# Performance work log

Hardware: AMD Instinct MI355X
Metric: run time of the kernel (lower is better)

The kernel has to match this reference:

```python
import jax, jax.numpy as jnp
import numpy as np

NUM_GRAPHS = 1024
BN_EPS = 1e-5
NEG_SLOPE = 0.01


def _xavier(key, fan_in, fan_out):
    lim = float(np.sqrt(6.0 / (fan_in + fan_out)))
    return jax.random.uniform(key, (fan_in, fan_out), jnp.float32, -lim, lim)


def setup_inputs() -> dict:
    key = jax.random.key(0)
    ks = jax.random.split(key, 10)
    N, F, H, C, E = 100000, 128, 128, 10, 1600000
    x = jax.random.normal(ks[0], (N, F), jnp.float32)
    edge_index = jax.random.randint(ks[1], (2, E), 0, N, jnp.int64)
    batch = jnp.sort(jax.random.randint(ks[2], (N,), 0, NUM_GRAPHS, jnp.int64))
    return {
        "x": x,
        "W1a": _xavier(ks[3], F, H), "b1a": jnp.zeros((H,), jnp.float32),
        "W1b": _xavier(ks[4], H, H), "b1b": jnp.zeros((H,), jnp.float32),
        "g1": jnp.ones((H,), jnp.float32), "be1": jnp.zeros((H,), jnp.float32),
        "W2a": _xavier(ks[5], H, H), "b2a": jnp.zeros((H,), jnp.float32),
        "W2b": _xavier(ks[6], H, H), "b2b": jnp.zeros((H,), jnp.float32),
        "g2": jnp.ones((H,), jnp.float32), "be2": jnp.zeros((H,), jnp.float32),
        "fcW1": _xavier(ks[7], H, H), "fcb1": jnp.zeros((H,), jnp.float32),
        "fcW2": _xavier(ks[8], H, C), "fcb2": jnp.zeros((C,), jnp.float32),
        "edge_index": edge_index,
        "batch": batch,
    }


def _leaky(x):
    return jax.nn.leaky_relu(x, NEG_SLOPE)


def _gin_conv(x, src, dst, Wa, ba, Wb, bb, num_nodes):
    # scatter-add neighbor aggregation: out[i] = (1+eps)*x[i] + sum_{j->i} x[j], eps=0
    agg = jax.ops.segment_sum(x[src], dst, num_segments=num_nodes)
    h = x + agg
    h = _leaky(h @ Wa + ba)
    return h @ Wb + bb


def _batch_norm(x, gamma, beta):
    # training-mode BN over node dim (biased variance, as torch BatchNorm1d)
    m = jnp.mean(x, axis=0)
    v = jnp.mean(jnp.square(x - m), axis=0)
    return gamma * (x - m) * jax.lax.rsqrt(v + BN_EPS) + beta


def reference(x, W1a, b1a, W1b, b1b, g1, be1, W2a, b2a, W2b, b2b, g2, be2,
              fcW1, fcb1, fcW2, fcb2, edge_index, batch):
    N = x.shape[0]
    src, dst = edge_index[0], edge_index[1]
    h = _leaky(_gin_conv(x, src, dst, W1a, b1a, W1b, b1b, N))
    h = _batch_norm(h, g1, be1)
    h = _leaky(_gin_conv(h, src, dst, W2a, b2a, W2b, b2b, N))
    h = _batch_norm(h, g2, be2)
    # global_add_pool: segment-sum nodes into graphs
    hg = jax.ops.segment_sum(h, batch, num_segments=NUM_GRAPHS)  # [G, H]
    hg = _leaky(hg @ fcW1 + fcb1)
    logits = hg @ fcW2 + fcb2
    return jax.nn.log_softmax(logits, axis=-1)
```

## Files before the change

kernel.cpp:

```cpp
#include <hip/hip_runtime.h>
#include <hip/hip_bf16.h>

#define NUM_GRAPHS 1024
#define NCLS 10
#define BN_EPS 1e-5f
#define SLOPE 0.01f
#define PB 256
#define WN 64
#define CAP 1280
#define NBMAX 1600

typedef __attribute__((ext_vector_type(8))) short          bfrag;
typedef __attribute__((ext_vector_type(4))) float          ffrag;
typedef __attribute__((ext_vector_type(8))) unsigned short ushort8;

__device__ __forceinline__ float leaky(float v) { return v > 0.f ? v : SLOPE * v; }

__device__ __forceinline__ unsigned short f2bf(float f) {
    unsigned int u = __float_as_uint(f);
    unsigned int r = (u + 0x7fffu + ((u >> 16) & 1u)) >> 16;
    return (unsigned short)r;
}
__device__ __forceinline__ float bf2f(unsigned short u) {
    return __uint_as_float(((unsigned int)u) << 16);
}

__device__ __forceinline__ void load_lds16(const void* g, void* l) {
    __builtin_amdgcn_global_load_lds((const __attribute__((address_space(1))) void*)g,
                                     (__attribute__((address_space(3))) void*)l, 16, 0, 0);
}

__global__ __launch_bounds__(256)
void scatter_cvt_kernel(const int* __restrict__ src, const int* __restrict__ dst,
                        int* __restrict__ cursor, int* __restrict__ packedE,
                        int E, int chunk, int NB,
                        const float* __restrict__ x, unsigned short* __restrict__ xb, int nX,
                        const float* __restrict__ W0, const float* __restrict__ W1,
                        const float* __restrict__ W2, const float* __restrict__ W3,
                        unsigned short* __restrict__ WT)
{
    int b = blockIdx.x;
    int t = threadIdx.x;
    if (b < PB) {
        __shared__ int h[NBMAX];
        __shared__ int base[NBMAX];
        for (int i = t; i < NB; i += 256) h[i] = 0;
        __syncthreads();
        int e0 = b * chunk;
        int e1 = min(E, e0 + chunk);
        for (int e = e0 + t; e < e1; e += 256)
            atomicAdd(&h[dst[e] >> 6], 1);
        __syncthreads();
        for (int i = t; i < NB; i += 256) {
            int c = h[i];
            base[i] = c ? atomicAdd(&cursor[i], c) : 0;
            h[i] = 0;
        }
        __syncthreads();
        for (int e = e0 + t; e < e1; e += 256) {
            int d = dst[e];
            int s = src[e];
            int bk = d >> 6;
            int off = atomicAdd(&h[bk], 1) + base[bk];
            if (off < CAP) packedE[bk * CAP + off] = (s << 6) | (d & 63);
        }
        return;
    }
    b -= PB;
    if (b < 4) {
        const float* W = (b == 0) ? W0 : (b == 1) ? W1 : (b == 2) ? W2 : W3;
        unsigned short* O = WT + (size_t)b * 16384;
#pragma unroll
        for (int p = 0; p < 64; ++p) {
            int idx = p * 256 + t;
            int n = idx >> 7, k = idx & 127;
            O[n * 128 + k] = f2bf(W[k * 128 + n]);
        }
        return;
    }
    b -= 4;
    int i = (b * 256 + t) * 4;
    if (i + 3 < nX) {
        float4 f = *(const float4*)&x[i];
        unsigned short o0 = f2bf(f.x), o1 = f2bf(f.y), o2 = f2bf(f.z), o3 = f2bf(f.w);
        unsigned long long packed = (unsigned long long)o0 | ((unsigned long long)o1 << 16)
                                  | ((unsigned long long)o2 << 32) | ((unsigned long long)o3 << 48);
        *(unsigned long long*)&xb[i] = packed;
    } else if (i < nX) {
        for (int j = i; j < nX; ++j) xb[j] = f2bf(x[j]);
    }
}

template<bool AFFINE>
__global__ __launch_bounds__(256)
void gather_win(const unsigned short* __restrict__ X, const int* __restrict__ cursor,
                const int* __restrict__ packedE,
                const float* __restrict__ bnsum, const float* __restrict__ bnsq,
                const float* __restrict__ g, const float* __restrict__ be,
                unsigned short* __restrict__ out, int N)
{
    __shared__ int   raw[CAP];
    __shared__ int   lst[CAP];
    __shared__ int   hist[WN];
    __shared__ int   offs[WN];
    __shared__ int   cur[WN];
    __shared__ float Af[128], Bf[128];

    const int k    = blockIdx.x >> 1;
    const int half = blockIdx.x & 1;
    const int t = threadIdx.x;

    if (t < WN) hist[t] = 0;
    if (AFFINE && t < 128) {
        float invN = 1.f / (float)N;
        float mean = bnsum[t] * invN;
        float var  = bnsq[t] * invN - mean * mean;
        float a = g[t] * rsqrtf(var + BN_EPS);
        Af[t] = a;
        Bf[t] = be[t] - a * mean;
    }
    __syncthreads();

    int cnt = cursor[k];
    if (cnt > CAP) cnt = CAP;
    const int* pe = packedE + (size_t)k * CAP;
    for (int i = t; i < cnt; i += 256) {
        int p = pe[i];
        raw[i] = p;
        atomicAdd(&hist[p & 63], 1);
    }
    __syncthreads();
    if (t < 64) {
        int v = hist[t];
        int x = v;
#pragma unroll
        for (int off = 1; off < 64; off <<= 1) {
            int y = __shfl_up(x, off, 64);
            if (t >= off) x += y;
        }
        offs[t] = x - v;
        cur[t]  = x - v;
    }
    __syncthreads();
    for (int i = t; i < cnt; i += 256) {
        int p = raw[i];
        int slot = atomicAdd(&cur[p & 63], 1);
        lst[slot] = p >> 6;
    }
    __syncthreads();

    const int grp = t >> 4;
    const int c8  = (t & 15) * 8;
#pragma unroll
    for (int pass = 0; pass < 2; ++pass) {
        int n = half * 32 + pass * 16 + grp;
        int node = k * WN + n;
        if (node >= N) continue;
        float acc[8];
        {
            ushort8 xv = *(const ushort8*)&X[(size_t)node * 128 + c8];
#pragma unroll
            for (int j = 0; j < 8; ++j) acc[j] = bf2f(xv[j]);
        }
        int s0 = offs[n];
        int dg = hist[n];
        int s1 = s0 + dg;
        int i = s0;
        for (; i + 1 < s1; i += 2) {
            int j0 = lst[i], j1 = lst[i + 1];
            ushort8 u0 = *(const ushort8*)&X[(size_t)j0 * 128 + c8];
            ushort8 u1 = *(const ushort8*)&X[(size_t)j1 * 128 + c8];
#pragma unroll
            for (int j = 0; j < 8; ++j) acc[j] += bf2f(u0[j]) + bf2f(u1[j]);
        }
        if (i < s1) {
            int j0 = lst[i];
            ushort8 u0 = *(const ushort8*)&X[(size_t)j0 * 128 + c8];
#pragma unroll
            for (int j = 0; j < 8; ++j) acc[j] += bf2f(u0[j]);
        }
        ushort8 o;
        if (AFFINE) {
            float cf = (float)(dg + 1);
#pragma unroll
            for (int j = 0; j < 8; ++j)
                o[j] = f2bf(fmaf(Af[c8 + j], acc[j], cf * Bf[c8 + j]));
        } else {
#pragma unroll
            for (int j = 0; j < 8; ++j) o[j] = f2bf(acc[j]);
        }
        *(ushort8*)&out[(size_t)node * 128 + c8] = o;
    }
}

template<bool STATS>
__global__ __launch_bounds__(256)
void gemm_mfma(const unsigned short* __restrict__ A, const unsigned short* __restrict__ WT,
               const float* __restrict__ bias, unsigned short* __restrict__ Out,
               float* __restrict__ stat_sum, float* __restrict__ stat_sq,
               const unsigned short* __restrict__ zeroPad, int N)
{
    __shared__ unsigned short As[128 * 128];
    __shared__ unsigned short Ws[128 * 128];
    __shared__ float sred[256];

    const int t = threadIdx.x;
    const int row0 = blockIdx.x * 128;

#pragma unroll
    for (int p = 0; p < 8; ++p) {
        int s  = p * 256 + t;
        int r  = s >> 4;
        int gp = s & 15;
        int g  = gp ^ (r & 7);
        int gr = row0 + r;
        const unsigned short* ga = (gr < N) ? &A[(size_t)gr * 128 + g * 8] : zeroPad;
        load_lds16(ga, &As[s * 8]);
        load_lds16(&WT[r * 128 + g * 8], &Ws[s * 8]);
    }
    __syncthreads();

    const int wave = t >> 6;
    const int lane = t & 63;
    const int m    = lane & 15;
    const int quad = lane >> 4;

    ffrag acc[2][8];
#pragma unroll
    for (int rt = 0; rt < 2; ++rt)
#pragma unroll
        for (int ct = 0; ct < 8; ++ct) {
            ffrag z = {0.f, 0.f, 0.f, 0.f};
            acc[rt][ct] = z;
        }

#pragma unroll
    for (int ks = 0; ks < 4; ++ks) {
        int kc = ks * 4 + quad;
        bfrag b[8];
#pragma unroll
        for (int ct = 0; ct < 8; ++ct) {
            int n = ct * 16 + m;
            b[ct] = *(const bfrag*)&Ws[(n * 16 + (kc ^ (n & 7))) * 8];
        }
        bfrag a0, a1;
        {
            int r = wave * 32 + m;
            a0 = *(const bfrag*)&As[(r * 16 + (kc ^ (r & 7))) * 8];
        }
        {
            int r = wave * 32 + 16 + m;
            a1 = *(const bfrag*)&As[(r * 16 + (kc ^ (r & 7))) * 8];
        }
#pragma unroll
        for (int ct = 0; ct < 8; ++ct) {
            acc[0][ct] = __builtin_amdgcn_mfma_f32_16x16x32_bf16(a0, b[ct], acc[0][ct], 0, 0, 0);
            acc[1][ct] = __builtin_amdgcn_mfma_f32_16x16x32_bf16(a1, b[ct], acc[1][ct], 0, 0, 0);
        }
    }

    float bv[8];
#pragma unroll
    for (int ct = 0; ct < 8; ++ct) bv[ct] = bias[ct * 16 + m];

    float colsum[8], colsq[8];
#pragma unroll
    for (int ct = 0; ct < 8; ++ct) { colsum[ct] = 0.f; colsq[ct] = 0.f; }

    __syncthreads();
    unsigned short* tw = &As[wave * 32 * 128];
#pragma unroll
    for (int rt = 0; rt < 2; ++rt) {
#pragma unroll
        for (int reg = 0; reg < 4; ++reg) {
            int rl = rt * 16 + quad * 4 + reg;
            bool valid = (row0 + wave * 32 + rl) < N;
#pragma unroll
            for (int ct = 0; ct < 8; ++ct) {
                float v = leaky(acc[rt][ct][reg] + bv[ct]);
                tw[rl * 128 + ct * 16 + m] = f2bf(v);
                if (STATS && valid) { colsum[ct] += v; colsq[ct] += v * v; }
            }
        }
    }
    __syncthreads();
#pragma unroll
    for (int p = 0; p < 8; ++p) {
        int li = p * 64 + lane;
        int rl = li >> 4;
        int cg = (li & 15) * 8;
        int r = row0 + wave * 32 + rl;
        if (r < N)
            *(ushort8*)&Out[(size_t)r * 128 + cg] = *(const ushort8*)&tw[rl * 128 + cg];
    }

    if (STATS) {
        __syncthreads();
        if (t < 128) { sred[t] = 0.f; sred[128 + t] = 0.f; }
        __syncthreads();
#pragma unroll
        for (int ct = 0; ct < 8; ++ct) {
            atomicAdd(&sred[ct * 16 + m], colsum[ct]);
            atomicAdd(&sred[128 + ct * 16 + m], colsq[ct]);
        }
        __syncthreads();
        if (t < 128) {
            atomicAdd(&stat_sum[t], sred[t]);
            atomicAdd(&stat_sq[t], sred[128 + t]);
        }
    }
}

__device__ __forceinline__ int lower_bound(const int* b, int n, int v)
{
    int lo = 0, hi = n;
    while (lo < hi) { int mid = (lo + hi) >> 1; if (b[mid] < v) lo = mid + 1; else hi = mid; }
    return lo;
}

__global__ __launch_bounds__(128)
void pool_head(const unsigned short* __restrict__ Hn, const int* __restrict__ batch,
               const float* __restrict__ bnsum, const float* __restrict__ bnsq,
               const float* __restrict__ g2, const float* __restrict__ be2,
               const float* __restrict__ fcW1, const float* __restrict__ fcb1,
               const float* __restrict__ fcW2, const float* __restrict__ fcb2,
               float* __restrict__ out, int N)
{
    int g = blockIdx.x;
    int t = threadIdx.x;
    __shared__ int bounds[2];
    __shared__ float row[128];
    __shared__ float z1[128];
    if (t < 2) bounds[t] = lower_bound(batch, N, g + t);
    float invN = 1.f / (float)N;
    float mean = bnsum[t] * invN;
    float var  = bnsq[t] * invN - mean * mean;
    float a2 = g2[t] * rsqrtf(var + BN_EPS);
    float b2 = be2[t] - a2 * mean;
    __syncthreads();
    int ss = bounds[0], se = bounds[1];
    float acc = 0.f;
    for (int i = ss; i < se; ++i) acc += bf2f(Hn[(size_t)i * 128 + t]);
    float cnt = (float)(se - ss);
    row[t] = fmaf(a2, acc, cnt * b2);
    __syncthreads();
    float a1 = fcb1[t];
#pragma unroll 8
    for (int k = 0; k < 128; ++k) a1 = fmaf(row[k], fcW1[(size_t)k * 128 + t], a1);
    z1[t] = leaky(a1);
    __syncthreads();
    if (t < 64) {
        float lg[NCLS];
#pragma unroll
        for (int c = 0; c < NCLS; ++c) {
            float p = z1[t] * fcW2[t * NCLS + c] + z1[t + 64] * fcW2[(t + 64) * NCLS + c];
#pragma unroll
            for (int off = 32; off > 0; off >>= 1) p += __shfl_down(p, off, 64);
            if (t == 0) lg[c] = p + fcb2[c];
        }
        if (t == 0) {
            float m = lg[0];
#pragma unroll
            for (int c = 1; c < NCLS; ++c) m = fmaxf(m, lg[c]);
            float s = 0.f;
#pragma unroll
            for (int c = 0; c < NCLS; ++c) s += expf(lg[c] - m);
            float lse = logf(s);
#pragma unroll
            for (int c = 0; c < NCLS; ++c) out[(size_t)g * NCLS + c] = lg[c] - m - lse;
        }
    }
}

extern "C" void kernel_launch(void* const* d_in, const int* in_sizes, int n_in,
                              void* d_out, int out_size, void* d_ws, size_t ws_size,
                              hipStream_t stream)
{
    const float* x    = (const float*)d_in[0];
    const float* W1a  = (const float*)d_in[1];
    const float* b1a  = (const float*)d_in[2];
    const float* W1b  = (const float*)d_in[3];
    const float* b1b  = (const float*)d_in[4];
    const float* g1   = (const float*)d_in[5];
    const float* be1  = (const float*)d_in[6];
    const float* W2a  = (const float*)d_in[7];
    const float* b2a  = (const float*)d_in[8];
    const float* W2b  = (const float*)d_in[9];
    const float* b2b  = (const float*)d_in[10];
    const float* g2   = (const float*)d_in[11];
    const float* be2  = (const float*)d_in[12];
    const float* fcW1 = (const float*)d_in[13];
    const float* fcb1 = (const float*)d_in[14];
    const float* fcW2 = (const float*)d_in[15];
    const float* fcb2 = (const float*)d_in[16];
    const int*   edge = (const int*)d_in[17];
    const int*   batch= (const int*)d_in[18];

    const int N = in_sizes[0] / 128;
    const int E = in_sizes[17] / 2;
    const int* src = edge;
    const int* dst = edge + E;
    const size_t NH = (size_t)N * 128;
    const int NB = (N + WN - 1) / WN;
    const int chunk = (E + PB - 1) / PB;

    int*   cursor = (int*)d_ws;
    float* stats  = (float*)(cursor + 2048);
    float* sum1   = stats;
    float* sq1    = stats + 128;
    float* sum2   = stats + 256;
    float* sq2    = stats + 384;
    unsigned short* zeroPad = (unsigned short*)(stats + 512);
    int*   packedE = (int*)(stats + 640);
    unsigned short* xb   = (unsigned short*)(packedE + ((size_t)NBMAX * CAP));
    unsigned short* bufA = xb + NH;
    unsigned short* bufB = bufA + NH;
    unsigned short* wt   = bufB + NH;
    unsigned short* wt1a = wt;
    unsigned short* wt1b = wt + 16384;
    unsigned short* wt2a = wt + 32768;
    unsigned short* wt2b = wt + 49152;

    const int cvtBlocks  = (int)((NH / 4 + 255) / 256);
    const int gemmBlocks = (N + 127) / 128;

    hipMemsetAsync(d_ws, 0, 2048 * sizeof(int) + 640 * sizeof(float), stream);

    scatter_cvt_kernel<<<PB + 4 + cvtBlocks, 256, 0, stream>>>(
        src, dst, cursor, packedE, E, chunk, NB,
        x, xb, (int)NH, W1a, W1b, W2a, W2b, wt);

    gather_win<false><<<NB * 2, 256, 0, stream>>>(xb, cursor, packedE,
                                                  nullptr, nullptr, nullptr, nullptr, bufA, N);
    gemm_mfma<false><<<gemmBlocks, 256, 0, stream>>>(bufA, wt1a, b1a, bufB,
                                                     nullptr, nullptr, zeroPad, N);
    gemm_mfma<true><<<gemmBlocks, 256, 0, stream>>>(bufB, wt1b, b1b, bufA,
                                                    sum1, sq1, zeroPad, N);

    gather_win<true><<<NB * 2, 256, 0, stream>>>(bufA, cursor, packedE,
                                                 sum1, sq1, g1, be1, bufB, N);
    gemm_mfma<false><<<gemmBlocks, 256, 0, stream>>>(bufB, wt2a, b2a, bufA,
                                                     nullptr, nullptr, zeroPad, N);
    gemm_mfma<true><<<gemmBlocks, 256, 0, stream>>>(bufA, wt2b, b2b, bufB,
                                                    sum2, sq2, zeroPad, N);

    pool_head<<<NUM_GRAPHS, 128, 0, stream>>>(bufB, batch, sum2, sq2, g2, be2,
                                              fcW1, fcb1, fcW2, fcb2, (float*)d_out, N);
}
```

Measured before the change: 434.1 us.

## Fuse both GIN MLP GEMMs into one kernel keeping the hidden tile in LDS

Each GIN conv's two 128x128 GEMMs now run in one kernel. The leaky-ReLU output of the first GEMM is written back, swizzled, into the A tile in shared memory and reused directly as the input of the second GEMM. This removes one global write and one global read of the N x 128 bf16 intermediate per conv, plus one kernel launch per conv. In exchange, LDS per block grows with a second weight tile, which lowers how many blocks fit per CU, and some barriers are dropped on the assumption that each wave only touches its own rows.

Measured after the change: 455.9 us. +5.0%, slower.

```diff
diff --git a/kernel.cpp b/kernel.cpp
--- a/kernel.cpp
+++ b/kernel.cpp
@@ -193,15 +193,17 @@
     }
 }
 
-template<bool STATS>
 __global__ __launch_bounds__(256)
-void gemm_mfma(const unsigned short* __restrict__ A, const unsigned short* __restrict__ WT,
-               const float* __restrict__ bias, unsigned short* __restrict__ Out,
-               float* __restrict__ stat_sum, float* __restrict__ stat_sq,
-               const unsigned short* __restrict__ zeroPad, int N)
+void conv_fused(const unsigned short* __restrict__ A,
+                const unsigned short* __restrict__ WT1, const float* __restrict__ b1,
+                const unsigned short* __restrict__ WT2, const float* __restrict__ b2,
+                unsigned short* __restrict__ Out,
+                float* __restrict__ stat_sum, float* __restrict__ stat_sq,
+                const unsigned short* __restrict__ zeroPad, int N)
 {
     __shared__ unsigned short As[128 * 128];
-    __shared__ unsigned short Ws[128 * 128];
+    __shared__ unsigned short W1s[128 * 128];
+    __shared__ unsigned short W2s[128 * 128];
     __shared__ float sred[256];
 
     const int t = threadIdx.x;
@@ -216,7 +218,8 @@
         int gr = row0 + r;
         const unsigned short* ga = (gr < N) ? &A[(size_t)gr * 128 + g * 8] : zeroPad;
         load_lds16(ga, &As[s * 8]);
-        load_lds16(&WT[r * 128 + g * 8], &Ws[s * 8]);
+        load_lds16(&WT1[r * 128 + g * 8], &W1s[s * 8]);
+        load_lds16(&WT2[r * 128 + g * 8], &W2s[s * 8]);
     }
     __syncthreads();
 
@@ -241,7 +244,7 @@
 #pragma unroll
         for (int ct = 0; ct < 8; ++ct) {
             int n = ct * 16 + m;
-            b[ct] = *(const bfrag*)&Ws[(n * 16 + (kc ^ (n & 7))) * 8];
+            b[ct] = *(const bfrag*)&W1s[(n * 16 + (kc ^ (n & 7))) * 8];
         }
         bfrag a0, a1;
         {
@@ -259,15 +262,65 @@
         }
     }
 
+    {
+        float bv[8];
+#pragma unroll
+        for (int ct = 0; ct < 8; ++ct) bv[ct] = b1[ct * 16 + m];
+#pragma unroll
+        for (int rt = 0; rt < 2; ++rt) {
+#pragma unroll
+            for (int reg = 0; reg < 4; ++reg) {
+                int rl = wave * 32 + rt * 16 + quad * 4 + reg;
+#pragma unroll
+                for (int ct = 0; ct < 8; ++ct) {
+                    int c = ct * 16 + m;
+                    float v = leaky(acc[rt][ct][reg] + bv[ct]);
+                    As[(rl * 16 + ((c >> 3) ^ (rl & 7))) * 8 + (c & 7)] = f2bf(v);
+                }
+            }
+        }
+    }
+
+#pragma unroll
+    for (int rt = 0; rt < 2; ++rt)
+#pragma unroll
+        for (int ct = 0; ct < 8; ++ct) {
+            ffrag z = {0.f, 0.f, 0.f, 0.f};
+            acc[rt][ct] = z;
+        }
+#pragma unroll
+    for (int ks = 0; ks < 4; ++ks) {
+        int kc = ks * 4 + quad;
+        bfrag b[8];
+#pragma unroll
+        for (int ct = 0; ct < 8; ++ct) {
+            int n = ct * 16 + m;
+            b[ct] = *(const bfrag*)&W2s[(n * 16 + (kc ^ (n & 7))) * 8];
+        }
+        bfrag a0, a1;
+        {
+            int r = wave * 32 + m;
+            a0 = *(const bfrag*)&As[(r * 16 + (kc ^ (r & 7))) * 8];
+        }
+        {
+            int r = wave * 32 + 16 + m;
+            a1 = *(const bfrag*)&As[(r * 16 + (kc ^ (r & 7))) * 8];
+        }
+#pragma unroll
+        for (int ct = 0; ct < 8; ++ct) {
+            acc[0][ct] = __builtin_amdgcn_mfma_f32_16x16x32_bf16(a0, b[ct], acc[0][ct], 0, 0, 0);
+            acc[1][ct] = __builtin_amdgcn_mfma_f32_16x16x32_bf16(a1, b[ct], acc[1][ct], 0, 0, 0);
+        }
+    }
+
     float bv[8];
 #pragma unroll
-    for (int ct = 0; ct < 8; ++ct) bv[ct] = bias[ct * 16 + m];
+    for (int ct = 0; ct < 8; ++ct) bv[ct] = b2[ct * 16 + m];
 
     float colsum[8], colsq[8];
 #pragma unroll
     for (int ct = 0; ct < 8; ++ct) { colsum[ct] = 0.f; colsq[ct] = 0.f; }
 
-    __syncthreads();
     unsigned short* tw = &As[wave * 32 * 128];
 #pragma unroll
     for (int rt = 0; rt < 2; ++rt) {
@@ -279,11 +332,10 @@
             for (int ct = 0; ct < 8; ++ct) {
                 float v = leaky(acc[rt][ct][reg] + bv[ct]);
                 tw[rl * 128 + ct * 16 + m] = f2bf(v);
-                if (STATS && valid) { colsum[ct] += v; colsq[ct] += v * v; }
+                if (valid) { colsum[ct] += v; colsq[ct] += v * v; }
             }
         }
     }
-    __syncthreads();
 #pragma unroll
     for (int p = 0; p < 8; ++p) {
         int li = p * 64 + lane;
@@ -294,20 +346,18 @@
             *(ushort8*)&Out[(size_t)r * 128 + cg] = *(const ushort8*)&tw[rl * 128 + cg];
     }
 
-    if (STATS) {
-        __syncthreads();
-        if (t < 128) { sred[t] = 0.f; sred[128 + t] = 0.f; }
-        __syncthreads();
-#pragma unroll
-        for (int ct = 0; ct < 8; ++ct) {
-            atomicAdd(&sred[ct * 16 + m], colsum[ct]);
-            atomicAdd(&sred[128 + ct * 16 + m], colsq[ct]);
-        }
-        __syncthreads();
-        if (t < 128) {
-            atomicAdd(&stat_sum[t], sred[t]);
-            atomicAdd(&stat_sq[t], sred[128 + t]);
-        }
+    __syncthreads();
+    if (t < 128) { sred[t] = 0.f; sred[128 + t] = 0.f; }
+    __syncthreads();
+#pragma unroll
+    for (int ct = 0; ct < 8; ++ct) {
+        atomicAdd(&sred[ct * 16 + m], colsum[ct]);
+        atomicAdd(&sred[128 + ct * 16 + m], colsq[ct]);
+    }
+    __syncthreads();
+    if (t < 128) {
+        atomicAdd(&stat_sum[t], sred[t]);
+        atomicAdd(&stat_sq[t], sred[128 + t]);
     }
 }
 
@@ -432,17 +482,13 @@
 
     gather_win<false><<<NB * 2, 256, 0, stream>>>(xb, cursor, packedE,
                                                   nullptr, nullptr, nullptr, nullptr, bufA, N);
-    gemm_mfma<false><<<gemmBlocks, 256, 0, stream>>>(bufA, wt1a, b1a, bufB,
-                                                     nullptr, nullptr, zeroPad, N);
-    gemm_mfma<true><<<gemmBlocks, 256, 0, stream>>>(bufB, wt1b, b1b, bufA,
-                                                    sum1, sq1, zeroPad, N);
-
-    gather_win<true><<<NB * 2, 256, 0, stream>>>(bufA, cursor, packedE,
-                                                 sum1, sq1, g1, be1, bufB, N);
-    gemm_mfma<false><<<gemmBlocks, 256, 0, stream>>>(bufB, wt2a, b2a, bufA,
-                                                     nullptr, nullptr, zeroPad, N);
-    gemm_mfma<true><<<gemmBlocks, 256, 0, stream>>>(bufA, wt2b, b2b, bufB,
-                                                    sum2, sq2, zeroPad, N);
+    conv_fused<<<gemmBlocks, 256, 0, stream>>>(bufA, wt1a, b1a, wt1b, b1b, bufB,
+                                               sum1, sq1, zeroPad, N);
+
+    gather_win<true><<<NB * 2, 256, 0, stream>>>(bufB, cursor, packedE,
+                                                 sum1, sq1, g1, be1, bufA, N);
+    conv_fused<<<gemmBlocks, 256, 0, stream>>>(bufA, wt2a, b2a, wt2b, b2b, bufB,
+                                               sum2, sq2, zeroPad, N);
 
     pool_head<<<NUM_GRAPHS, 128, 0, stream>>>(bufB, batch, sum2, sq2, g2, be2,
                                               fcW1, fcb1, fcW2, fcb2, (float*)d_out, N);
```
